# Performance work log

Hardware: AMD Instinct MI355X
Metric: run time of the kernel (lower is better)

Reference implementation:

```python
import jax, jax.numpy as jnp
import numpy as np

SEQ_LEN = 512
PRED_LEN = 336
N_PTS = 8
N_PARAMS = 2
N_SLOTS = N_PTS + 1
B = 8192


def setup_inputs() -> dict:
    key = jax.random.key(0)
    k_x, k1, k2, k3, k4 = jax.random.split(key, 5)
    s_pts = 1.0 / np.sqrt(SEQ_LEN)
    inp = {
        "x": jax.random.normal(k_x, (B, SEQ_LEN), dtype=jnp.float32),
        # pts_lin: Linear(seq_len, n_pts * pred_len)
        "W_pts": jax.random.uniform(k1, (N_PTS * PRED_LEN, SEQ_LEN), jnp.float32, -s_pts, s_pts),
        "b_pts": jax.random.uniform(k2, (N_PTS * PRED_LEN,), jnp.float32, -s_pts, s_pts),
        # component_lin: Linear(seq_len, n_slots * n_params)
        "W_comp": jax.random.uniform(k3, (N_SLOTS * N_PARAMS, SEQ_LEN), jnp.float32, -s_pts, s_pts),
        "b_comp": jax.random.uniform(k4, (N_SLOTS * N_PARAMS,), jnp.float32, -s_pts, s_pts),
    }
    return inp


def reference(x, W_pts, b_pts, W_comp, b_comp):
    # x: (B, seq_len)
    last_val = x[:, -1:]                       # (B, 1)
    xc = x - last_val

    # _generate_points: linear -> argmax over pred_len -> sort
    logits = xc @ W_pts.T + b_pts              # (B, n_pts*pred_len)
    logits = logits.reshape(-1, N_PTS, PRED_LEN)
    pts = jnp.sort(jnp.argmax(logits, axis=-1).astype(jnp.int32), axis=-1)  # (B, n_pts)

    # _generate_component_params
    params = (xc @ W_comp.T + b_comp).reshape(-1, N_SLOTS, N_PARAMS)  # (B, n_slots, 2)

    # concrete _generate: piecewise-linear component per slot over the horizon
    t = jnp.arange(PRED_LEN, dtype=jnp.float32)                     # (pred_len,)
    pts_data = params[..., 0:1] * t + params[..., 1:2]              # (B, n_slots, pred_len)

    # _combine_by_pts: pad pts with 0 and pred_len, build dynamic segment mask
    b = x.shape[0]
    zeros = jnp.zeros((b, 1), dtype=jnp.int32)
    full = jnp.full((b, 1), PRED_LEN, dtype=jnp.int32)
    pts_ext = jnp.concatenate([zeros, pts, full], axis=-1)          # (B, n_slots+1)
    start_ids = pts_ext[:, :N_SLOTS, None]                          # (B, n_slots, 1)
    end_ids = pts_ext[:, 1:, None]                                  # (B, n_slots, 1)
    ti = jnp.arange(PRED_LEN, dtype=jnp.int32)                      # (pred_len,)
    mask = (ti >= start_ids) & (ti < end_ids)                       # (B, n_slots, pred_len)
    result = jnp.sum(jnp.where(mask, pts_data, 0.0), axis=-2)       # (B, pred_len)

    return result + last_val
```

## Files before the change

### kernel.cpp

```cpp
#include <hip/hip_runtime.h>

#define SEQ    512
#define PRED   336
#define NPTS   8
#define NG     8
#define NCOMP  18
#define BATCH  8192
#define TAU    1e-4f
#define NEGBIG (-3.402823466e+38f)
#define BIGI   0x7fffffff

typedef __bf16 bf16x8 __attribute__((ext_vector_type(8)));
typedef float  f32x4  __attribute__((ext_vector_type(4)));

__device__ __forceinline__ void gload_lds16(const __bf16* g, __bf16* l) {
  __builtin_amdgcn_global_load_lds(
      (const __attribute__((address_space(1))) unsigned int*)(const void*)g,
      (__attribute__((address_space(3))) unsigned int*)(void*)l, 16, 0, 0);
}

__global__ __launch_bounds__(256) void k_pack(
    const float* __restrict__ x, const float* __restrict__ Wp,
    const float* __restrict__ Wc, const float* __restrict__ bc,
    __bf16* __restrict__ Apk, __bf16* __restrict__ Bhl,
    float* __restrict__ params)
{
  const int lane = threadIdx.x & 63, wid = threadIdx.x >> 6;
  const int b = blockIdx.x;
  if (b < BATCH / 4) {
    const int row = b * 4 + wid;
    const float* src = x + (size_t)row * SEQ;
    const float last = src[SEQ - 1];
    float4 u0 = *(const float4*)&src[lane * 8];
    float4 u1 = *(const float4*)&src[lane * 8 + 4];
    float xc[8] = {u0.x - last, u0.y - last, u0.z - last, u0.w - last,
                   u1.x - last, u1.y - last, u1.z - last, u1.w - last};
    bf16x8 h, l;
#pragma unroll
    for (int j = 0; j < 8; ++j) {
      __bf16 hb = (__bf16)xc[j];
      float rest = xc[j] - (float)hb;
      h[j] = hb; l[j] = (__bf16)rest;
    }
    const int H = lane >> 2, lk = lane & 3;
    const size_t base = ((size_t)(row >> 4) * 32 + H * 2) * 512
                      + (size_t)(lk * 16 + (row & 15)) * 8;
    *(bf16x8*)&Apk[base]       = h;
    *(bf16x8*)&Apk[base + 512] = l;

    float pd[NCOMP];
#pragma unroll
    for (int s = 0; s < NCOMP; ++s) {
      const float* w = Wc + (size_t)s * SEQ + lane * 8;
      float4 w0 = *(const float4*)(w);
      float4 w1 = *(const float4*)(w + 4);
      float a = 0.f;
      a = fmaf(xc[0], w0.x, a); a = fmaf(xc[1], w0.y, a);
      a = fmaf(xc[2], w0.z, a); a = fmaf(xc[3], w0.w, a);
      a = fmaf(xc[4], w1.x, a); a = fmaf(xc[5], w1.y, a);
      a = fmaf(xc[6], w1.z, a); a = fmaf(xc[7], w1.w, a);
      pd[s] = a;
    }
#pragma unroll
    for (int d = 1; d < 64; d <<= 1)
#pragma unroll
      for (int s = 0; s < NCOMP; ++s) pd[s] += __shfl_xor(pd[s], d);
    if (lane < NCOMP) params[(size_t)row * NCOMP + lane] = pd[lane] + bc[lane];
  } else {
    const int row = (b - BATCH / 4) * 4 + wid;
    const int g = row / 384, local = row - g * 384;
    bf16x8 h, l;
    if (local < PRED) {
      const float* src = Wp + (size_t)(g * PRED + local) * SEQ;
      float4 u0 = *(const float4*)&src[lane * 8];
      float4 u1 = *(const float4*)&src[lane * 8 + 4];
      float v[8] = {u0.x, u0.y, u0.z, u0.w, u1.x, u1.y, u1.z, u1.w};
#pragma unroll
      for (int j = 0; j < 8; ++j) {
        __bf16 hb = (__bf16)v[j];
        float rest = v[j] - (float)hb;
        h[j] = hb; l[j] = (__bf16)rest;
      }
    } else {
#pragma unroll
      for (int j = 0; j < 8; ++j) { h[j] = (__bf16)0.f; l[j] = (__bf16)0.f; }
    }
    const int kb = lane >> 2, j0 = (lane & 3) * 8;
    __bf16* dst = Bhl + (size_t)row * 1024;
    const size_t base = (size_t)(kb * 64 + j0);
    *(bf16x8*)&dst[base]      = h;
    *(bf16x8*)&dst[base + 32] = l;
  }
}

__global__ __launch_bounds__(256, 3) void k1_mfma(
    const __bf16* __restrict__ Apk, const __bf16* __restrict__ Bhl,
    const float* __restrict__ bp,
    float* __restrict__ t1v, int* __restrict__ t1i,
    float* __restrict__ t2v, int* __restrict__ t2i)
{
  __shared__ __bf16 sbuf[2][8192];
  const int tid  = threadIdx.x;
  const int lane = tid & 63, wid = tid >> 6;
  const int bid  = blockIdx.x;
  const int v    = (bid & 7) * 192 + (bid >> 3);
  const int mt   = v / 24;
  const int nt   = v % 24;
  const int row0 = mt * 128;
  const int ncol0 = nt * 128;

  const __bf16* gsrc[4];
  int dsti[4];
#pragma unroll
  for (int i = 0; i < 4; ++i) {
    const int c = i * 256 + tid;
    dsti[i] = c * 8;
    const int c2 = c & 511;
    const int lk = c2 >> 7, col = c2 & 127;
    gsrc[i] = Bhl + (size_t)(ncol0 + col) * 1024 + lk * 8 + ((c < 512) ? 0 : 32);
  }
  const __bf16* abase[2];
#pragma unroll
  for (int m = 0; m < 2; ++m)
    abase[m] = Apk + (size_t)(mt * 8 + wid * 2 + m) * 16384 + (size_t)lane * 8;

  const int lr = lane & 15, lk2 = lane >> 4;
  const int fb = lk2 * 1024 + lr * 8;

  f32x4 acc[2][8];
#pragma unroll
  for (int m = 0; m < 2; ++m)
#pragma unroll
    for (int n = 0; n < 8; ++n) acc[m][n] = (f32x4){0.f, 0.f, 0.f, 0.f};

  bf16x8 ah[2][2], al[2][2];

#define STAGE(H, WP) do { \
  _Pragma("unroll") \
  for (int i_ = 0; i_ < 4; ++i_) gload_lds16(gsrc[i_] + (H) * 64, (WP) + dsti[i_]); \
} while (0)
#define ALOAD(H, S) do { \
  _Pragma("unroll") \
  for (int m_ = 0; m_ < 2; ++m_) { \
    ah[S][m_] = *(const bf16x8*)(abase[m_] + (H) * 1024); \
    al[S][m_] = *(const bf16x8*)(abase[m_] + (H) * 1024 + 512); } \
} while (0)

  STAGE(0, &sbuf[0][0]);
  ALOAD(0, 0);
  __syncthreads();

#pragma unroll
  for (int H = 0; H < 16; ++H) {
    const int cur = H & 1;
    if (H < 15) { STAGE(H + 1, &sbuf[cur ^ 1][0]); ALOAD(H + 1, cur ^ 1); }
    const __bf16* rs = &sbuf[cur][0];
    bf16x8 bh[8], bl[8];
#pragma unroll
    for (int n = 0; n < 8; ++n) {
      bh[n] = *(const bf16x8*)&rs[fb + n * 128];
      bl[n] = *(const bf16x8*)&rs[4096 + fb + n * 128];
    }
#pragma unroll
    for (int n = 0; n < 8; ++n)
#pragma unroll
      for (int m = 0; m < 2; ++m) {
        acc[m][n] = __builtin_amdgcn_mfma_f32_16x16x32_bf16(ah[cur][m], bh[n], acc[m][n], 0, 0, 0);
        acc[m][n] = __builtin_amdgcn_mfma_f32_16x16x32_bf16(ah[cur][m], bl[n], acc[m][n], 0, 0, 0);
        acc[m][n] = __builtin_amdgcn_mfma_f32_16x16x32_bf16(al[cur][m], bh[n], acc[m][n], 0, 0, 0);
      }
    __syncthreads();
  }
#undef STAGE
#undef ALOAD

  const int g = nt / 3, colg0 = (nt % 3) * 128;
  float bias[8];
#pragma unroll
  for (int n = 0; n < 8; ++n) {
    const int col = colg0 + n * 16 + lr;
    bias[n] = (col < PRED) ? bp[g * PRED + col] : NEGBIG;
  }

#define GT(a,ia,b,ib) ((a) > (b) || ((a) == (b) && (ia) < (ib)))
#pragma unroll
  for (int m = 0; m < 2; ++m)
#pragma unroll
    for (int r = 0; r < 4; ++r) {
      float v1 = NEGBIG, v2 = NEGBIG; int i1 = BIGI, i2 = BIGI;
#pragma unroll
      for (int n = 0; n < 8; ++n) {
        const float vv = acc[m][n][r] + bias[n];
        const int col = colg0 + n * 16 + lr;
        if (vv > v1)      { v2 = v1; i2 = i1; v1 = vv; i1 = col; }
        else if (vv > v2) { v2 = vv; i2 = col; }
      }
#pragma unroll
      for (int d = 1; d < 16; d <<= 1) {
        const float o1 = __shfl_xor(v1, d), o2 = __shfl_xor(v2, d);
        const int   p1 = __shfl_xor(i1, d), p2 = __shfl_xor(i2, d);
        if (GT(o1, p1, v1, i1)) {
          if (GT(v1, i1, o2, p2)) { v2 = v1; i2 = i1; }
          else                    { v2 = o2; i2 = p2; }
          v1 = o1; i1 = p1;
        } else if (GT(o1, p1, v2, i2)) { v2 = o1; i2 = p1; }
      }
      if (lr == 0) {
        const int rowg = row0 + wid * 32 + m * 16 + lk2 * 4 + r;
        const int o = rowg * 24 + nt;
        t1v[o] = v1; t1i[o] = i1; t2v[o] = v2; t2i[o] = i2;
      }
    }
#undef GT
}

__global__ __launch_bounds__(256) void k23_out(
    const float* __restrict__ x, const float* __restrict__ Wp,
    const float* __restrict__ bp, const float* __restrict__ params,
    const float* __restrict__ t1v, const int* __restrict__ t1i,
    const float* __restrict__ t2v, const int* __restrict__ t2i,
    float* __restrict__ out)
{
  const int lane = threadIdx.x & 63;
  const int wid  = threadIdx.x >> 6;
  const int row  = blockIdx.x * 4 + wid;

  float v[6]; int ix[6];
  float v1 = NEGBIG; int i1 = BIGI; bool flag = false;
#pragma unroll
  for (int s = 0; s < 6; ++s) { v[s] = NEGBIG; ix[s] = BIGI; }
  if (lane < 8) {
    const int base = row * 24 + lane * 3;
#pragma unroll
    for (int t = 0; t < 3; ++t) {
      v[2 * t]     = t1v[base + t]; ix[2 * t]     = t1i[base + t];
      v[2 * t + 1] = t2v[base + t]; ix[2 * t + 1] = t2i[base + t];
    }
#pragma unroll
    for (int s = 0; s < 6; ++s)
      if (v[s] > v1 || (v[s] == v1 && ix[s] < i1)) { v1 = v[s]; i1 = ix[s]; }
    int cnt = 0;
#pragma unroll
    for (int s = 0; s < 6; ++s) cnt += (v[s] >= v1 - TAU) ? 1 : 0;
    flag = (cnt >= 2);
  }

  int p[8];
#pragma unroll
  for (int j = 0; j < 8; ++j) p[j] = __shfl(i1, j);

  unsigned long long mb = __ballot(flag);
  if (mb) {
    const float* xr = x + (size_t)row * SEQ;
    const float last = xr[SEQ - 1];
    double xd[8];
    {
      float4 a0 = *(const float4*)&xr[lane * 8];
      float4 a1 = *(const float4*)&xr[lane * 8 + 4];
      xd[0]=(double)(a0.x-last); xd[1]=(double)(a0.y-last); xd[2]=(double)(a0.z-last); xd[3]=(double)(a0.w-last);
      xd[4]=(double)(a1.x-last); xd[5]=(double)(a1.y-last); xd[6]=(double)(a1.z-last); xd[7]=(double)(a1.w-last);
    }
    while (mb) {
      const int L = (int)__ffsll((long long)mb) - 1; mb &= mb - 1;
      const float bv1 = __shfl(v1, L);
      double bb = -1e300; int bi = BIGI;
#pragma unroll
      for (int s = 0; s < 6; ++s) {
        const float vs = __shfl(v[s], L);
        const int   is = __shfl(ix[s], L);
        if (vs >= bv1 - TAU) {
          const float* w = Wp + ((size_t)L * PRED + is) * SEQ + lane * 8;
          float4 w0 = *(const float4*)w, w1 = *(const float4*)(w + 4);
          double t = 0.0;
          t += xd[0]*(double)w0.x + xd[1]*(double)w0.y + xd[2]*(double)w0.z + xd[3]*(double)w0.w;
          t += xd[4]*(double)w1.x + xd[5]*(double)w1.y + xd[6]*(double)w1.z + xd[7]*(double)w1.w;
#pragma unroll
          for (int d = 1; d < 64; d <<= 1) t += __shfl_xor(t, d);
          t += (double)bp[L * PRED + is];
          if (t > bb || (t == bb && is < bi)) { bb = t; bi = is; }
        }
      }
      p[L] = bi;
    }
  }

#define CSW(a,b) { int lo_ = min(p[a], p[b]); int hi_ = max(p[a], p[b]); p[a] = lo_; p[b] = hi_; }
  CSW(0,1) CSW(2,3) CSW(4,5) CSW(6,7)
  CSW(0,2) CSW(1,3) CSW(4,6) CSW(5,7)
  CSW(1,2) CSW(5,6)
  CSW(0,4) CSW(1,5) CSW(2,6) CSW(3,7)
  CSW(2,4) CSW(3,5)
  CSW(1,2) CSW(3,4) CSW(5,6)
#undef CSW

  const float last = x[(size_t)row * SEQ + (SEQ - 1)];
  float pd[NCOMP];
#pragma unroll
  for (int s = 0; s < NCOMP; ++s) pd[s] = params[(size_t)row * NCOMP + s];

  for (int t = lane; t < PRED; t += 64) {
    int slot = 0;
#pragma unroll
    for (int j = 0; j < 8; ++j) slot += (p[j] <= t) ? 1 : 0;
    out[(size_t)row * PRED + t] = fmaf(pd[slot * 2], (float)t, pd[slot * 2 + 1]) + last;
  }
}

extern "C" void kernel_launch(void* const* d_in, const int* in_sizes, int n_in,
                              void* d_out, int out_size, void* d_ws, size_t ws_size,
                              hipStream_t stream)
{
  const float* x  = (const float*)d_in[0];
  const float* Wp = (const float*)d_in[1];
  const float* bp = (const float*)d_in[2];
  const float* Wc = (const float*)d_in[3];
  const float* bc = (const float*)d_in[4];
  float* out = (float*)d_out;

  char* w = (char*)d_ws;
  __bf16* Apk = (__bf16*)w;  w += (size_t)BATCH * 1024 * 2;
  __bf16* Bhl = (__bf16*)w;  w += (size_t)3072 * 1024 * 2;
  float* t1v  = (float*)w;   w += (size_t)BATCH * 24 * 4;
  int*   t1i  = (int*)w;     w += (size_t)BATCH * 24 * 4;
  float* t2v  = (float*)w;   w += (size_t)BATCH * 24 * 4;
  int*   t2i  = (int*)w;     w += (size_t)BATCH * 24 * 4;
  float* params = (float*)w; w += (size_t)BATCH * NCOMP * 4;

  hipLaunchKernelGGL(k_pack, dim3(BATCH / 4 + 3072 / 4), dim3(256), 0, stream,
                     x, Wp, Wc, bc, Apk, Bhl, params);
  hipLaunchKernelGGL(k1_mfma, dim3(1536), dim3(256), 0, stream,
                     Apk, Bhl, bp, t1v, t1i, t2v, t2i);
  hipLaunchKernelGGL(k23_out, dim3(BATCH / 4), dim3(256), 0, stream,
                     x, Wp, bp, params, t1v, t1i, t2v, t2i, out);
}
```

Baseline: 121.2 us.

## Split GEMM tile across eight waves with one M-subtile per wave

The 128x128 MFMA tile is now computed by 8 waves (512 threads), each owning a single 16-row M subtile, instead of 4 waves owning two subtiles each. This halves accumulator and A-fragment registers per wave and halves the per-thread global-to-LDS staging work, aiming for more resident waves to hide latency. In exchange, every wave re-reads the full B fragments from LDS, so LDS read traffic per tile doubles, and the larger block makes barriers more costly.

```diff
diff --git a/kernel.cpp b/kernel.cpp
--- a/kernel.cpp
+++ b/kernel.cpp
@@ -93,7 +93,7 @@
   }
 }
 
-__global__ __launch_bounds__(256, 3) void k1_mfma(
+__global__ __launch_bounds__(512, 4) void k1_mfma(
     const __bf16* __restrict__ Apk, const __bf16* __restrict__ Bhl,
     const float* __restrict__ bp,
     float* __restrict__ t1v, int* __restrict__ t1i,
@@ -109,41 +109,32 @@
   const int row0 = mt * 128;
   const int ncol0 = nt * 128;
 
-  const __bf16* gsrc[4];
-  int dsti[4];
-#pragma unroll
-  for (int i = 0; i < 4; ++i) {
-    const int c = i * 256 + tid;
-    dsti[i] = c * 8;
-    const int c2 = c & 511;
-    const int lk = c2 >> 7, col = c2 & 127;
-    gsrc[i] = Bhl + (size_t)(ncol0 + col) * 1024 + lk * 8 + ((c < 512) ? 0 : 32);
-  }
-  const __bf16* abase[2];
-#pragma unroll
-  for (int m = 0; m < 2; ++m)
-    abase[m] = Apk + (size_t)(mt * 8 + wid * 2 + m) * 16384 + (size_t)lane * 8;
+  const __bf16* gsrc[2];
+  int dsti[2];
+  {
+    const int lk = (tid & 511) >> 7, col = tid & 127;
+    const __bf16* p = Bhl + (size_t)(ncol0 + col) * 1024 + lk * 8;
+    gsrc[0] = p;        dsti[0] = tid * 8;
+    gsrc[1] = p + 32;   dsti[1] = (tid + 512) * 8;
+  }
+  const __bf16* abase = Apk + (size_t)(mt * 8 + wid) * 16384 + (size_t)lane * 8;
 
   const int lr = lane & 15, lk2 = lane >> 4;
   const int fb = lk2 * 1024 + lr * 8;
 
-  f32x4 acc[2][8];
-#pragma unroll
-  for (int m = 0; m < 2; ++m)
-#pragma unroll
-    for (int n = 0; n < 8; ++n) acc[m][n] = (f32x4){0.f, 0.f, 0.f, 0.f};
-
-  bf16x8 ah[2][2], al[2][2];
+  f32x4 acc[8];
+#pragma unroll
+  for (int n = 0; n < 8; ++n) acc[n] = (f32x4){0.f, 0.f, 0.f, 0.f};
+
+  bf16x8 ah[2], al[2];
 
 #define STAGE(H, WP) do { \
   _Pragma("unroll") \
-  for (int i_ = 0; i_ < 4; ++i_) gload_lds16(gsrc[i_] + (H) * 64, (WP) + dsti[i_]); \
+  for (int i_ = 0; i_ < 2; ++i_) gload_lds16(gsrc[i_] + (H) * 64, (WP) + dsti[i_]); \
 } while (0)
 #define ALOAD(H, S) do { \
-  _Pragma("unroll") \
-  for (int m_ = 0; m_ < 2; ++m_) { \
-    ah[S][m_] = *(const bf16x8*)(abase[m_] + (H) * 1024); \
-    al[S][m_] = *(const bf16x8*)(abase[m_] + (H) * 1024 + 512); } \
+  ah[S] = *(const bf16x8*)(abase + (H) * 1024); \
+  al[S] = *(const bf16x8*)(abase + (H) * 1024 + 512); \
 } while (0)
 
   STAGE(0, &sbuf[0][0]);
@@ -162,13 +153,11 @@
       bl[n] = *(const bf16x8*)&rs[4096 + fb + n * 128];
     }
 #pragma unroll
-    for (int n = 0; n < 8; ++n)
-#pragma unroll
-      for (int m = 0; m < 2; ++m) {
-        acc[m][n] = __builtin_amdgcn_mfma_f32_16x16x32_bf16(ah[cur][m], bh[n], acc[m][n], 0, 0, 0);
-        acc[m][n] = __builtin_amdgcn_mfma_f32_16x16x32_bf16(ah[cur][m], bl[n], acc[m][n], 0, 0, 0);
-        acc[m][n] = __builtin_amdgcn_mfma_f32_16x16x32_bf16(al[cur][m], bh[n], acc[m][n], 0, 0, 0);
-      }
+    for (int n = 0; n < 8; ++n) {
+      acc[n] = __builtin_amdgcn_mfma_f32_16x16x32_bf16(ah[cur], bh[n], acc[n], 0, 0, 0);
+      acc[n] = __builtin_amdgcn_mfma_f32_16x16x32_bf16(ah[cur], bl[n], acc[n], 0, 0, 0);
+      acc[n] = __builtin_amdgcn_mfma_f32_16x16x32_bf16(al[cur], bh[n], acc[n], 0, 0, 0);
+    }
     __syncthreads();
   }
 #undef STAGE
@@ -184,33 +173,31 @@
 
 #define GT(a,ia,b,ib) ((a) > (b) || ((a) == (b) && (ia) < (ib)))
 #pragma unroll
-  for (int m = 0; m < 2; ++m)
-#pragma unroll
-    for (int r = 0; r < 4; ++r) {
-      float v1 = NEGBIG, v2 = NEGBIG; int i1 = BIGI, i2 = BIGI;
-#pragma unroll
-      for (int n = 0; n < 8; ++n) {
-        const float vv = acc[m][n][r] + bias[n];
-        const int col = colg0 + n * 16 + lr;
-        if (vv > v1)      { v2 = v1; i2 = i1; v1 = vv; i1 = col; }
-        else if (vv > v2) { v2 = vv; i2 = col; }
-      }
-#pragma unroll
-      for (int d = 1; d < 16; d <<= 1) {
-        const float o1 = __shfl_xor(v1, d), o2 = __shfl_xor(v2, d);
-        const int   p1 = __shfl_xor(i1, d), p2 = __shfl_xor(i2, d);
-        if (GT(o1, p1, v1, i1)) {
-          if (GT(v1, i1, o2, p2)) { v2 = v1; i2 = i1; }
-          else                    { v2 = o2; i2 = p2; }
-          v1 = o1; i1 = p1;
-        } else if (GT(o1, p1, v2, i2)) { v2 = o1; i2 = p1; }
-      }
-      if (lr == 0) {
-        const int rowg = row0 + wid * 32 + m * 16 + lk2 * 4 + r;
-        const int o = rowg * 24 + nt;
-        t1v[o] = v1; t1i[o] = i1; t2v[o] = v2; t2i[o] = i2;
-      }
-    }
+  for (int r = 0; r < 4; ++r) {
+    float v1 = NEGBIG, v2 = NEGBIG; int i1 = BIGI, i2 = BIGI;
+#pragma unroll
+    for (int n = 0; n < 8; ++n) {
+      const float vv = acc[n][r] + bias[n];
+      const int col = colg0 + n * 16 + lr;
+      if (vv > v1)      { v2 = v1; i2 = i1; v1 = vv; i1 = col; }
+      else if (vv > v2) { v2 = vv; i2 = col; }
+    }
+#pragma unroll
+    for (int d = 1; d < 16; d <<= 1) {
+      const float o1 = __shfl_xor(v1, d), o2 = __shfl_xor(v2, d);
+      const int   p1 = __shfl_xor(i1, d), p2 = __shfl_xor(i2, d);
+      if (GT(o1, p1, v1, i1)) {
+        if (GT(v1, i1, o2, p2)) { v2 = v1; i2 = i1; }
+        else                    { v2 = o2; i2 = p2; }
+        v1 = o1; i1 = p1;
+      } else if (GT(o1, p1, v2, i2)) { v2 = o1; i2 = p1; }
+    }
+    if (lr == 0) {
+      const int rowg = row0 + wid * 16 + lk2 * 4 + r;
+      const int o = rowg * 24 + nt;
+      t1v[o] = v1; t1i[o] = i1; t2v[o] = v2; t2i[o] = i2;
+    }
+  }
 #undef GT
 }
 
@@ -328,7 +315,7 @@
 
   hipLaunchKernelGGL(k_pack, dim3(BATCH / 4 + 3072 / 4), dim3(256), 0, stream,
                      x, Wp, Wc, bc, Apk, Bhl, params);
-  hipLaunchKernelGGL(k1_mfma, dim3(1536), dim3(256), 0, stream,
+  hipLaunchKernelGGL(k1_mfma, dim3(1536), dim3(512), 0, stream,
                      Apk, Bhl, bp, t1v, t1i, t2v, t2i);
   hipLaunchKernelGGL(k23_out, dim3(BATCH / 4), dim3(256), 0, stream,
                      x, Wp, bp, params, t1v, t1i, t2v, t2i, out);
```

New measurement: 124.3 us. 2.6% more time.

## Use single bf16 GEMM with top-3 candidates and fp64 rescoring instead of split-bf16

Applied to the files above, without the earlier changes.

Drops the hi/lo bf16 split of both operands, so the argmax GEMM runs one MFMA per tile instead of three and packs half as much data. To keep argmax exact despite the coarser logits, the epilogue now keeps a top-3 per tile. The rescoring kernel checks candidates against a much wider tolerance in fp64, and falls back to a full fp64 rescan of a tile when its third candidate is near the best. The risk is more rescoring work, and possible mismatches if bf16 error ever exceeds the tolerance.

```diff
diff --git a/kernel.cpp b/kernel.cpp
--- a/kernel.cpp
+++ b/kernel.cpp
@@ -6,7 +6,7 @@
 #define NG     8
 #define NCOMP  18
 #define BATCH  8192
-#define TAU    1e-4f
+#define TAU    0.03f
 #define NEGBIG (-3.402823466e+38f)
 #define BIGI   0x7fffffff
 
@@ -22,7 +22,7 @@
 __global__ __launch_bounds__(256) void k_pack(
     const float* __restrict__ x, const float* __restrict__ Wp,
     const float* __restrict__ Wc, const float* __restrict__ bc,
-    __bf16* __restrict__ Apk, __bf16* __restrict__ Bhl,
+    __bf16* __restrict__ Apk, __bf16* __restrict__ Bh,
     float* __restrict__ params)
 {
   const int lane = threadIdx.x & 63, wid = threadIdx.x >> 6;
@@ -35,18 +35,13 @@
     float4 u1 = *(const float4*)&src[lane * 8 + 4];
     float xc[8] = {u0.x - last, u0.y - last, u0.z - last, u0.w - last,
                    u1.x - last, u1.y - last, u1.z - last, u1.w - last};
-    bf16x8 h, l;
-#pragma unroll
-    for (int j = 0; j < 8; ++j) {
-      __bf16 hb = (__bf16)xc[j];
-      float rest = xc[j] - (float)hb;
-      h[j] = hb; l[j] = (__bf16)rest;
-    }
+    bf16x8 h;
+#pragma unroll
+    for (int j = 0; j < 8; ++j) h[j] = (__bf16)xc[j];
     const int H = lane >> 2, lk = lane & 3;
-    const size_t base = ((size_t)(row >> 4) * 32 + H * 2) * 512
+    const size_t base = (size_t)(row >> 4) * 8192 + H * 512
                       + (size_t)(lk * 16 + (row & 15)) * 8;
-    *(bf16x8*)&Apk[base]       = h;
-    *(bf16x8*)&Apk[base + 512] = l;
+    *(bf16x8*)&Apk[base] = h;
 
     float pd[NCOMP];
 #pragma unroll
@@ -69,37 +64,28 @@
   } else {
     const int row = (b - BATCH / 4) * 4 + wid;
     const int g = row / 384, local = row - g * 384;
-    bf16x8 h, l;
+    bf16x8 h;
     if (local < PRED) {
       const float* src = Wp + (size_t)(g * PRED + local) * SEQ;
       float4 u0 = *(const float4*)&src[lane * 8];
       float4 u1 = *(const float4*)&src[lane * 8 + 4];
       float v[8] = {u0.x, u0.y, u0.z, u0.w, u1.x, u1.y, u1.z, u1.w};
 #pragma unroll
-      for (int j = 0; j < 8; ++j) {
-        __bf16 hb = (__bf16)v[j];
-        float rest = v[j] - (float)hb;
-        h[j] = hb; l[j] = (__bf16)rest;
-      }
+      for (int j = 0; j < 8; ++j) h[j] = (__bf16)v[j];
     } else {
 #pragma unroll
-      for (int j = 0; j < 8; ++j) { h[j] = (__bf16)0.f; l[j] = (__bf16)0.f; }
-    }
-    const int kb = lane >> 2, j0 = (lane & 3) * 8;
-    __bf16* dst = Bhl + (size_t)row * 1024;
-    const size_t base = (size_t)(kb * 64 + j0);
-    *(bf16x8*)&dst[base]      = h;
-    *(bf16x8*)&dst[base + 32] = l;
+      for (int j = 0; j < 8; ++j) h[j] = (__bf16)0.f;
+    }
+    *(bf16x8*)&Bh[(size_t)row * 512 + lane * 8] = h;
   }
 }
 
 __global__ __launch_bounds__(256, 3) void k1_mfma(
-    const __bf16* __restrict__ Apk, const __bf16* __restrict__ Bhl,
+    const __bf16* __restrict__ Apk, const __bf16* __restrict__ Bh,
     const float* __restrict__ bp,
-    float* __restrict__ t1v, int* __restrict__ t1i,
-    float* __restrict__ t2v, int* __restrict__ t2i)
+    float* __restrict__ tV, int* __restrict__ tI)
 {
-  __shared__ __bf16 sbuf[2][8192];
+  __shared__ __bf16 sbuf[2][4096];
   const int tid  = threadIdx.x;
   const int lane = tid & 63, wid = tid >> 6;
   const int bid  = blockIdx.x;
@@ -109,20 +95,19 @@
   const int row0 = mt * 128;
   const int ncol0 = nt * 128;
 
-  const __bf16* gsrc[4];
-  int dsti[4];
-#pragma unroll
-  for (int i = 0; i < 4; ++i) {
+  const __bf16* gsrc[2];
+  int dsti[2];
+#pragma unroll
+  for (int i = 0; i < 2; ++i) {
     const int c = i * 256 + tid;
     dsti[i] = c * 8;
-    const int c2 = c & 511;
-    const int lk = c2 >> 7, col = c2 & 127;
-    gsrc[i] = Bhl + (size_t)(ncol0 + col) * 1024 + lk * 8 + ((c < 512) ? 0 : 32);
+    const int col = c & 127, lk = c >> 7;
+    gsrc[i] = Bh + (size_t)(ncol0 + col) * 512 + lk * 8;
   }
   const __bf16* abase[2];
 #pragma unroll
   for (int m = 0; m < 2; ++m)
-    abase[m] = Apk + (size_t)(mt * 8 + wid * 2 + m) * 16384 + (size_t)lane * 8;
+    abase[m] = Apk + (size_t)(mt * 8 + wid * 2 + m) * 8192 + (size_t)lane * 8;
 
   const int lr = lane & 15, lk2 = lane >> 4;
   const int fb = lk2 * 1024 + lr * 8;
@@ -133,17 +118,16 @@
 #pragma unroll
     for (int n = 0; n < 8; ++n) acc[m][n] = (f32x4){0.f, 0.f, 0.f, 0.f};
 
-  bf16x8 ah[2][2], al[2][2];
+  bf16x8 ah[2][2];
 
 #define STAGE(H, WP) do { \
   _Pragma("unroll") \
-  for (int i_ = 0; i_ < 4; ++i_) gload_lds16(gsrc[i_] + (H) * 64, (WP) + dsti[i_]); \
+  for (int i_ = 0; i_ < 2; ++i_) gload_lds16(gsrc[i_] + (H) * 32, (WP) + dsti[i_]); \
 } while (0)
 #define ALOAD(H, S) do { \
   _Pragma("unroll") \
-  for (int m_ = 0; m_ < 2; ++m_) { \
-    ah[S][m_] = *(const bf16x8*)(abase[m_] + (H) * 1024); \
-    al[S][m_] = *(const bf16x8*)(abase[m_] + (H) * 1024 + 512); } \
+  for (int m_ = 0; m_ < 2; ++m_) \
+    ah[S][m_] = *(const bf16x8*)(abase[m_] + (H) * 512); \
 } while (0)
 
   STAGE(0, &sbuf[0][0]);
@@ -155,20 +139,14 @@
     const int cur = H & 1;
     if (H < 15) { STAGE(H + 1, &sbuf[cur ^ 1][0]); ALOAD(H + 1, cur ^ 1); }
     const __bf16* rs = &sbuf[cur][0];
-    bf16x8 bh[8], bl[8];
-#pragma unroll
-    for (int n = 0; n < 8; ++n) {
-      bh[n] = *(const bf16x8*)&rs[fb + n * 128];
-      bl[n] = *(const bf16x8*)&rs[4096 + fb + n * 128];
-    }
+    bf16x8 bh[8];
+#pragma unroll
+    for (int n = 0; n < 8; ++n) bh[n] = *(const bf16x8*)&rs[fb + n * 128];
 #pragma unroll
     for (int n = 0; n < 8; ++n)
 #pragma unroll
-      for (int m = 0; m < 2; ++m) {
+      for (int m = 0; m < 2; ++m)
         acc[m][n] = __builtin_amdgcn_mfma_f32_16x16x32_bf16(ah[cur][m], bh[n], acc[m][n], 0, 0, 0);
-        acc[m][n] = __builtin_amdgcn_mfma_f32_16x16x32_bf16(ah[cur][m], bl[n], acc[m][n], 0, 0, 0);
-        acc[m][n] = __builtin_amdgcn_mfma_f32_16x16x32_bf16(al[cur][m], bh[n], acc[m][n], 0, 0, 0);
-      }
     __syncthreads();
   }
 #undef STAGE
@@ -183,66 +161,68 @@
   }
 
 #define GT(a,ia,b,ib) ((a) > (b) || ((a) == (b) && (ia) < (ib)))
+#define INS(vv, ii) do { \
+  const float v_ = (vv); const int c_ = (ii); \
+  if (GT(v_, c_, v1, i1))      { v3 = v2; i3 = i2; v2 = v1; i2 = i1; v1 = v_; i1 = c_; } \
+  else if (GT(v_, c_, v2, i2)) { v3 = v2; i3 = i2; v2 = v_; i2 = c_; } \
+  else if (GT(v_, c_, v3, i3)) { v3 = v_; i3 = c_; } \
+} while (0)
+
 #pragma unroll
   for (int m = 0; m < 2; ++m)
 #pragma unroll
     for (int r = 0; r < 4; ++r) {
-      float v1 = NEGBIG, v2 = NEGBIG; int i1 = BIGI, i2 = BIGI;
-#pragma unroll
-      for (int n = 0; n < 8; ++n) {
-        const float vv = acc[m][n][r] + bias[n];
-        const int col = colg0 + n * 16 + lr;
-        if (vv > v1)      { v2 = v1; i2 = i1; v1 = vv; i1 = col; }
-        else if (vv > v2) { v2 = vv; i2 = col; }
-      }
+      float v1 = NEGBIG, v2 = NEGBIG, v3 = NEGBIG;
+      int i1 = BIGI, i2 = BIGI, i3 = BIGI;
+#pragma unroll
+      for (int n = 0; n < 8; ++n)
+        INS(acc[m][n][r] + bias[n], colg0 + n * 16 + lr);
 #pragma unroll
       for (int d = 1; d < 16; d <<= 1) {
-        const float o1 = __shfl_xor(v1, d), o2 = __shfl_xor(v2, d);
-        const int   p1 = __shfl_xor(i1, d), p2 = __shfl_xor(i2, d);
-        if (GT(o1, p1, v1, i1)) {
-          if (GT(v1, i1, o2, p2)) { v2 = v1; i2 = i1; }
-          else                    { v2 = o2; i2 = p2; }
-          v1 = o1; i1 = p1;
-        } else if (GT(o1, p1, v2, i2)) { v2 = o1; i2 = p1; }
+        const float o1 = __shfl_xor(v1, d), o2 = __shfl_xor(v2, d), o3 = __shfl_xor(v3, d);
+        const int   q1 = __shfl_xor(i1, d), q2 = __shfl_xor(i2, d), q3 = __shfl_xor(i3, d);
+        INS(o1, q1); INS(o2, q2); INS(o3, q3);
       }
       if (lr == 0) {
         const int rowg = row0 + wid * 32 + m * 16 + lk2 * 4 + r;
-        const int o = rowg * 24 + nt;
-        t1v[o] = v1; t1i[o] = i1; t2v[o] = v2; t2i[o] = i2;
+        const size_t o = ((size_t)rowg * 24 + nt) * 3;
+        tV[o] = v1; tV[o + 1] = v2; tV[o + 2] = v3;
+        tI[o] = i1; tI[o + 1] = i2; tI[o + 2] = i3;
       }
     }
+#undef INS
 #undef GT
 }
 
 __global__ __launch_bounds__(256) void k23_out(
     const float* __restrict__ x, const float* __restrict__ Wp,
     const float* __restrict__ bp, const float* __restrict__ params,
-    const float* __restrict__ t1v, const int* __restrict__ t1i,
-    const float* __restrict__ t2v, const int* __restrict__ t2i,
+    const float* __restrict__ tV, const int* __restrict__ tI,
     float* __restrict__ out)
 {
   const int lane = threadIdx.x & 63;
   const int wid  = threadIdx.x >> 6;
   const int row  = blockIdx.x * 4 + wid;
 
-  float v[6]; int ix[6];
-  float v1 = NEGBIG; int i1 = BIGI; bool flag = false;
-#pragma unroll
-  for (int s = 0; s < 6; ++s) { v[s] = NEGBIG; ix[s] = BIGI; }
+#define GT(a,ia,b,ib) ((a) > (b) || ((a) == (b) && (ia) < (ib)))
+  float cv[9]; int ci[9];
+#pragma unroll
+  for (int s = 0; s < 9; ++s) { cv[s] = NEGBIG; ci[s] = BIGI; }
+  float v1 = NEGBIG; int i1 = BIGI; int hid = 0; bool flag = false;
   if (lane < 8) {
-    const int base = row * 24 + lane * 3;
-#pragma unroll
-    for (int t = 0; t < 3; ++t) {
-      v[2 * t]     = t1v[base + t]; ix[2 * t]     = t1i[base + t];
-      v[2 * t + 1] = t2v[base + t]; ix[2 * t + 1] = t2i[base + t];
-    }
-#pragma unroll
-    for (int s = 0; s < 6; ++s)
-      if (v[s] > v1 || (v[s] == v1 && ix[s] < i1)) { v1 = v[s]; i1 = ix[s]; }
+    const size_t base = ((size_t)row * 24 + lane * 3) * 3;
+#pragma unroll
+    for (int s = 0; s < 9; ++s) { cv[s] = tV[base + s]; ci[s] = tI[base + s]; }
+#pragma unroll
+    for (int s = 0; s < 9; ++s)
+      if (GT(cv[s], ci[s], v1, i1)) { v1 = cv[s]; i1 = ci[s]; }
     int cnt = 0;
 #pragma unroll
-    for (int s = 0; s < 6; ++s) cnt += (v[s] >= v1 - TAU) ? 1 : 0;
-    flag = (cnt >= 2);
+    for (int s = 0; s < 9; ++s) cnt += (cv[s] >= v1 - TAU) ? 1 : 0;
+#pragma unroll
+    for (int t = 0; t < 3; ++t)
+      if (cv[t * 3 + 2] >= v1 - TAU) hid |= (1 << t);
+    flag = (cnt >= 2) || (hid != 0);
   }
 
   int p[8];
@@ -252,37 +232,50 @@
   unsigned long long mb = __ballot(flag);
   if (mb) {
     const float* xr = x + (size_t)row * SEQ;
-    const float last = xr[SEQ - 1];
+    const float lastx = xr[SEQ - 1];
     double xd[8];
     {
       float4 a0 = *(const float4*)&xr[lane * 8];
       float4 a1 = *(const float4*)&xr[lane * 8 + 4];
-      xd[0]=(double)(a0.x-last); xd[1]=(double)(a0.y-last); xd[2]=(double)(a0.z-last); xd[3]=(double)(a0.w-last);
-      xd[4]=(double)(a1.x-last); xd[5]=(double)(a1.y-last); xd[6]=(double)(a1.z-last); xd[7]=(double)(a1.w-last);
+      xd[0]=(double)(a0.x-lastx); xd[1]=(double)(a0.y-lastx); xd[2]=(double)(a0.z-lastx); xd[3]=(double)(a0.w-lastx);
+      xd[4]=(double)(a1.x-lastx); xd[5]=(double)(a1.y-lastx); xd[6]=(double)(a1.z-lastx); xd[7]=(double)(a1.w-lastx);
     }
     while (mb) {
       const int L = (int)__ffsll((long long)mb) - 1; mb &= mb - 1;
-      const float bv1 = __shfl(v1, L);
       double bb = -1e300; int bi = BIGI;
 #pragma unroll
-      for (int s = 0; s < 6; ++s) {
-        const float vs = __shfl(v[s], L);
-        const int   is = __shfl(ix[s], L);
-        if (vs >= bv1 - TAU) {
-          const float* w = Wp + ((size_t)L * PRED + is) * SEQ + lane * 8;
+      for (int s = 0; s < 9; ++s) {
+        const int is = __shfl(ci[s], L);
+        const float* w = Wp + ((size_t)L * PRED + is) * SEQ + lane * 8;
+        float4 w0 = *(const float4*)w, w1 = *(const float4*)(w + 4);
+        double t = 0.0;
+        t += xd[0]*(double)w0.x + xd[1]*(double)w0.y + xd[2]*(double)w0.z + xd[3]*(double)w0.w;
+        t += xd[4]*(double)w1.x + xd[5]*(double)w1.y + xd[6]*(double)w1.z + xd[7]*(double)w1.w;
+#pragma unroll
+        for (int d = 1; d < 64; d <<= 1) t += __shfl_xor(t, d);
+        t += (double)bp[L * PRED + is];
+        if (t > bb || (t == bb && is < bi)) { bb = t; bi = is; }
+      }
+      const int h = __shfl(hid, L);
+      for (int t3 = 0; t3 < 3; ++t3) {
+        if (!((h >> t3) & 1)) continue;
+        const int cend = min(t3 * 128 + 128, PRED);
+        for (int c = t3 * 128; c < cend; ++c) {
+          const float* w = Wp + ((size_t)L * PRED + c) * SEQ + lane * 8;
           float4 w0 = *(const float4*)w, w1 = *(const float4*)(w + 4);
           double t = 0.0;
           t += xd[0]*(double)w0.x + xd[1]*(double)w0.y + xd[2]*(double)w0.z + xd[3]*(double)w0.w;
           t += xd[4]*(double)w1.x + xd[5]*(double)w1.y + xd[6]*(double)w1.z + xd[7]*(double)w1.w;
 #pragma unroll
           for (int d = 1; d < 64; d <<= 1) t += __shfl_xor(t, d);
-          t += (double)bp[L * PRED + is];
-          if (t > bb || (t == bb && is < bi)) { bb = t; bi = is; }
+          t += (double)bp[L * PRED + c];
+          if (t > bb || (t == bb && c < bi)) { bb = t; bi = c; }
         }
       }
       p[L] = bi;
     }
   }
+#undef GT
 
 #define CSW(a,b) { int lo_ = min(p[a], p[b]); int hi_ = max(p[a], p[b]); p[a] = lo_; p[b] = hi_; }
   CSW(0,1) CSW(2,3) CSW(4,5) CSW(6,7)
@@ -318,18 +311,16 @@
   float* out = (float*)d_out;
 
   char* w = (char*)d_ws;
-  __bf16* Apk = (__bf16*)w;  w += (size_t)BATCH * 1024 * 2;
-  __bf16* Bhl = (__bf16*)w;  w += (size_t)3072 * 1024 * 2;
-  float* t1v  = (float*)w;   w += (size_t)BATCH * 24 * 4;
-  int*   t1i  = (int*)w;     w += (size_t)BATCH * 24 * 4;
-  float* t2v  = (float*)w;   w += (size_t)BATCH * 24 * 4;
-  int*   t2i  = (int*)w;     w += (size_t)BATCH * 24 * 4;
+  __bf16* Apk = (__bf16*)w;  w += (size_t)BATCH * SEQ * 2;
+  __bf16* Bh  = (__bf16*)w;  w += (size_t)3072 * SEQ * 2;
+  float* tV   = (float*)w;   w += (size_t)BATCH * 24 * 3 * 4;
+  int*   tI   = (int*)w;     w += (size_t)BATCH * 24 * 3 * 4;
   float* params = (float*)w; w += (size_t)BATCH * NCOMP * 4;
 
   hipLaunchKernelGGL(k_pack, dim3(BATCH / 4 + 3072 / 4), dim3(256), 0, stream,
-                     x, Wp, Wc, bc, Apk, Bhl, params);
+                     x, Wp, Wc, bc, Apk, Bh, params);
   hipLaunchKernelGGL(k1_mfma, dim3(1536), dim3(256), 0, stream,
-                     Apk, Bhl, bp, t1v, t1i, t2v, t2i);
+                     Apk, Bh, bp, tV, tI);
   hipLaunchKernelGGL(k23_out, dim3(BATCH / 4), dim3(256), 0, stream,
-                     x, Wp, bp, params, t1v, t1i, t2v, t2i, out);
-}
+                     x, Wp, bp, params, tV, tI, out);
+}
```

After: 234.2 us. 1.93x slower.
